# Kernel tuning notes

Hardware: AMD Instinct MI355X
Metric: run time of the kernel (lower is better)

Reference implementation:

```python
import jax, jax.numpy as jnp
import numpy as np

N_TOTAL = 2_000_000
B = 50_000
D_MODEL = 128
HIDDEN = 64


def setup_inputs() -> dict:
    key = jax.random.key(0)
    ks = jax.random.split(key, 5)
    h = jax.random.normal(ks[0], (N_TOTAL, D_MODEL), dtype=jnp.float32)
    segment_ids = jnp.sort(jax.random.randint(ks[1], (N_TOTAL,), 0, B, dtype=jnp.int32))
    # MLP params (Linear stores [out,in] in torch; we use [in,out] with x @ W)
    W1 = jax.random.normal(ks[2], (D_MODEL, HIDDEN), dtype=jnp.float32) * (1.0 / np.sqrt(D_MODEL))
    b1 = jnp.zeros((HIDDEN,), dtype=jnp.float32)
    W2 = jax.random.normal(ks[3], (HIDDEN, HIDDEN), dtype=jnp.float32) * (1.0 / np.sqrt(HIDDEN))
    b2 = jnp.zeros((HIDDEN,), dtype=jnp.float32)
    W3 = jax.random.normal(ks[4], (HIDDEN, 1), dtype=jnp.float32) * (1.0 / np.sqrt(HIDDEN))
    b3 = jnp.zeros((1,), dtype=jnp.float32)
    return {"h": h, "segment_ids": segment_ids, "num_segments": B,
            "W1": W1, "b1": b1, "W2": W2, "b2": b2, "W3": W3, "b3": b3}


def reference(h, segment_ids, num_segments, W1, b1, W2, b2, W3, b3):
    # Ragged mean pooling over atoms -> [B, d_model] (fused segment reduce)
    sums = jax.ops.segment_sum(h, segment_ids, num_segments=num_segments)
    counts = jax.ops.segment_sum(jnp.ones((h.shape[0],), h.dtype), segment_ids,
                                 num_segments=num_segments)
    pooled = sums / jnp.maximum(counts, 1.0)[:, None]  # [B, d_model]
    # 3-layer MLP with SiLU -> scalar per molecule
    x = jax.nn.silu(pooled @ W1 + b1)
    x = jax.nn.silu(x @ W2 + b2)
    scalar = (x @ W3 + b3)[:, 0]  # [B]
    return scalar
```

## Files before the change

kernel.cpp:

```cpp
#include <hip/hip_runtime.h>

#define D_MODEL 128
#define HIDDEN 64
#define WPB 8
#define NTHREADS (WPB * 64)
#define NBLOCKS 512
#define W1_STRIDE 132
#define W2_STRIDE 68

__global__ void seg_bounds_kernel(const int* __restrict__ seg, int n, int B,
                                  int* __restrict__ seg_start) {
  int i = blockIdx.x * blockDim.x + threadIdx.x;
  if (i >= n) return;
  int s = seg[i];
  if (i == 0) {
    for (int t = 0; t <= s; ++t) seg_start[t] = 0;
  } else {
    int p = seg[i - 1];
    for (int t = p + 1; t <= s; ++t) seg_start[t] = i;
  }
  if (i == n - 1) {
    for (int t = s + 1; t <= B; ++t) seg_start[t] = n;
  }
}

__device__ __forceinline__ float silu(float x) {
  return x / (1.0f + __expf(-x));
}

__global__ __launch_bounds__(NTHREADS, 4) void pool_mlp_kernel(
    const float* __restrict__ h, const int* __restrict__ seg_start,
    const float* __restrict__ W1, const float* __restrict__ b1,
    const float* __restrict__ W2, const float* __restrict__ b2,
    const float* __restrict__ W3, const float* __restrict__ b3,
    float* __restrict__ out, int B) {
  __shared__ float sW1T[HIDDEN * W1_STRIDE];
  __shared__ float sW2T[HIDDEN * W2_STRIDE];
  __shared__ float pooled_lds[WPB][D_MODEL];
  __shared__ float x1_lds[WPB][HIDDEN];

  const int tid = threadIdx.x;

#pragma unroll
  for (int i = tid; i < (D_MODEL * HIDDEN) / 4; i += NTHREADS) {
    float4 v = reinterpret_cast<const float4*>(W1)[i];
    int k = i >> 4;
    int j = (4 * i) & (HIDDEN - 1);
    sW1T[(j + 0) * W1_STRIDE + k] = v.x;
    sW1T[(j + 1) * W1_STRIDE + k] = v.y;
    sW1T[(j + 2) * W1_STRIDE + k] = v.z;
    sW1T[(j + 3) * W1_STRIDE + k] = v.w;
  }
#pragma unroll
  for (int i = tid; i < (HIDDEN * HIDDEN) / 4; i += NTHREADS) {
    float4 v = reinterpret_cast<const float4*>(W2)[i];
    int k = i >> 4;
    int j = (4 * i) & (HIDDEN - 1);
    sW2T[(j + 0) * W2_STRIDE + k] = v.x;
    sW2T[(j + 1) * W2_STRIDE + k] = v.y;
    sW2T[(j + 2) * W2_STRIDE + k] = v.z;
    sW2T[(j + 3) * W2_STRIDE + k] = v.w;
  }
  __syncthreads();

  const int wave = tid >> 6;
  const int lane = tid & 63;

  const float b1l = b1[lane];
  const float b2l = b2[lane];
  const float w3l = W3[lane];
  const float b3l = b3[0];

  const int G = gridDim.x * WPB;
  const int g = blockIdx.x * WPB + wave;
  const int base = B / G;
  const int rem = B - base * G;
  const int my_cnt = base + (g < rem ? 1 : 0);
  const int my_s0 = g * base + (g < rem ? g : rem);
  if (my_cnt == 0) return;

  const int half = lane >> 5;
  const int l32 = lane & 63 & 31;
  const float4* __restrict__ hv = reinterpret_cast<const float4*>(h);
  const float4* __restrict__ pv =
      reinterpret_cast<const float4*>(&pooled_lds[wave][0]);
  const float4* __restrict__ x1v =
      reinterpret_cast<const float4*>(&x1_lds[wave][0]);
  const float4* __restrict__ w1v =
      reinterpret_cast<const float4*>(&sW1T[lane * W1_STRIDE]);
  const float4* __restrict__ w2v =
      reinterpret_cast<const float4*>(&sW2T[lane * W2_STRIDE]);

  int start = seg_start[my_s0];
  for (int si = 0; si < my_cnt; ++si) {
    const int s = my_s0 + si;
    const int end = seg_start[s + 1];
    const int cnt = end - start;

    float4 acc0 = make_float4(0.f, 0.f, 0.f, 0.f);
    float4 acc1 = make_float4(0.f, 0.f, 0.f, 0.f);
    int a = start + half;
    for (; a + 2 < end; a += 4) {
      float4 v0 = hv[a * 32 + l32];
      float4 v1 = hv[(a + 2) * 32 + l32];
      acc0.x += v0.x; acc0.y += v0.y; acc0.z += v0.z; acc0.w += v0.w;
      acc1.x += v1.x; acc1.y += v1.y; acc1.z += v1.z; acc1.w += v1.w;
    }
    if (a < end) {
      float4 v0 = hv[a * 32 + l32];
      acc0.x += v0.x; acc0.y += v0.y; acc0.z += v0.z; acc0.w += v0.w;
    }
    acc0.x += acc1.x; acc0.y += acc1.y; acc0.z += acc1.z; acc0.w += acc1.w;
    acc0.x += __shfl_xor(acc0.x, 32);
    acc0.y += __shfl_xor(acc0.y, 32);
    acc0.z += __shfl_xor(acc0.z, 32);
    acc0.w += __shfl_xor(acc0.w, 32);

    const float inv = 1.0f / (float)max(cnt, 1);
    if (half == 0) {
      float4 p = make_float4(acc0.x * inv, acc0.y * inv,
                             acc0.z * inv, acc0.w * inv);
      reinterpret_cast<float4*>(&pooled_lds[wave][0])[l32] = p;
    }
    __builtin_amdgcn_wave_barrier();

    float a1 = b1l;
#pragma unroll 8
    for (int t = 0; t < D_MODEL / 4; ++t) {
      float4 p = pv[t];
      float4 w = w1v[t];
      a1 = fmaf(p.x, w.x, a1);
      a1 = fmaf(p.y, w.y, a1);
      a1 = fmaf(p.z, w.z, a1);
      a1 = fmaf(p.w, w.w, a1);
    }
    const float x1 = silu(a1);
    x1_lds[wave][lane] = x1;
    __builtin_amdgcn_wave_barrier();

    float a2 = b2l;
#pragma unroll 8
    for (int t = 0; t < HIDDEN / 4; ++t) {
      float4 p = x1v[t];
      float4 w = w2v[t];
      a2 = fmaf(p.x, w.x, a2);
      a2 = fmaf(p.y, w.y, a2);
      a2 = fmaf(p.z, w.z, a2);
      a2 = fmaf(p.w, w.w, a2);
    }
    const float x2 = silu(a2);

    float prod = x2 * w3l;
#pragma unroll
    for (int off = 32; off >= 1; off >>= 1) {
      prod += __shfl_xor(prod, off);
    }
    if (lane == 0) out[s] = prod + b3l;

    start = end;
  }
}

extern "C" void kernel_launch(void* const* d_in, const int* in_sizes, int n_in,
                              void* d_out, int out_size, void* d_ws, size_t ws_size,
                              hipStream_t stream) {
  const float* h = (const float*)d_in[0];
  const int* seg = (const int*)d_in[1];
  const float* W1 = (const float*)d_in[3];
  const float* b1 = (const float*)d_in[4];
  const float* W2 = (const float*)d_in[5];
  const float* b2 = (const float*)d_in[6];
  const float* W3 = (const float*)d_in[7];
  const float* b3 = (const float*)d_in[8];
  float* out = (float*)d_out;

  const int n = in_sizes[1];
  const int B = out_size;

  int* seg_start = (int*)d_ws;

  {
    int threads = 256;
    int blocks = (n + threads - 1) / threads;
    seg_bounds_kernel<<<blocks, threads, 0, stream>>>(seg, n, B, seg_start);
  }
  {
    pool_mlp_kernel<<<NBLOCKS, NTHREADS, 0, stream>>>(
        h, seg_start, W1, b1, W2, b2, W3, b3, out, B);
  }
}
```

Before: 197.2 us.

## Batch four segments per MLP pass and prefetch next batch's atoms

Each wave now pools four segments into LDS, then runs the MLP over all four at once, so every W1/W2 weight read from LDS is reused across four segments. Before the MLP compute, it issues loads for the first atoms of the next batch so global memory latency overlaps the MLP math. The pooling inner loop is also unrolled to four independent float4 loads per iteration. The cost is more registers and LDS per wave, which could lower occupancy, plus clamped tail loads that fetch a few unused rows.

```diff
diff --git a/kernel.cpp b/kernel.cpp
--- a/kernel.cpp
+++ b/kernel.cpp
@@ -7,6 +7,7 @@
 #define NBLOCKS 512
 #define W1_STRIDE 132
 #define W2_STRIDE 68
+#define SEG_BATCH 4
 
 __global__ void seg_bounds_kernel(const int* __restrict__ seg, int n, int B,
                                   int* __restrict__ seg_start) {
@@ -27,17 +28,25 @@
 __device__ __forceinline__ float silu(float x) {
   return x / (1.0f + __expf(-x));
 }
+__device__ __forceinline__ float4 f4add(float4 a, float4 b) {
+  return make_float4(a.x + b.x, a.y + b.y, a.z + b.z, a.w + b.w);
+}
+__device__ __forceinline__ float wave_sum(float p) {
+#pragma unroll
+  for (int off = 32; off >= 1; off >>= 1) p += __shfl_xor(p, off);
+  return p;
+}
 
 __global__ __launch_bounds__(NTHREADS, 4) void pool_mlp_kernel(
     const float* __restrict__ h, const int* __restrict__ seg_start,
     const float* __restrict__ W1, const float* __restrict__ b1,
     const float* __restrict__ W2, const float* __restrict__ b2,
     const float* __restrict__ W3, const float* __restrict__ b3,
-    float* __restrict__ out, int B) {
+    float* __restrict__ out, int B, int n_atoms) {
   __shared__ float sW1T[HIDDEN * W1_STRIDE];
   __shared__ float sW2T[HIDDEN * W2_STRIDE];
-  __shared__ float pooled_lds[WPB][D_MODEL];
-  __shared__ float x1_lds[WPB][HIDDEN];
+  __shared__ float pooled_lds[WPB][SEG_BATCH][D_MODEL];
+  __shared__ float x1_lds[WPB][SEG_BATCH][HIDDEN];
 
   const int tid = threadIdx.x;
 
@@ -65,7 +74,6 @@
 
   const int wave = tid >> 6;
   const int lane = tid & 63;
-
   const float b1l = b1[lane];
   const float b2l = b2[lane];
   const float w3l = W3[lane];
@@ -80,84 +88,129 @@
   if (my_cnt == 0) return;
 
   const int half = lane >> 5;
-  const int l32 = lane & 63 & 31;
+  const int l32 = lane & 31;
   const float4* __restrict__ hv = reinterpret_cast<const float4*>(h);
-  const float4* __restrict__ pv =
-      reinterpret_cast<const float4*>(&pooled_lds[wave][0]);
-  const float4* __restrict__ x1v =
-      reinterpret_cast<const float4*>(&x1_lds[wave][0]);
   const float4* __restrict__ w1v =
       reinterpret_cast<const float4*>(&sW1T[lane * W1_STRIDE]);
   const float4* __restrict__ w2v =
       reinterpret_cast<const float4*>(&sW2T[lane * W2_STRIDE]);
 
+  float4 pf0, pf1, pf2, pf3;
+  bool have_pf = false;
+
   int start = seg_start[my_s0];
-  for (int si = 0; si < my_cnt; ++si) {
-    const int s = my_s0 + si;
-    const int end = seg_start[s + 1];
-    const int cnt = end - start;
-
-    float4 acc0 = make_float4(0.f, 0.f, 0.f, 0.f);
-    float4 acc1 = make_float4(0.f, 0.f, 0.f, 0.f);
-    int a = start + half;
-    for (; a + 2 < end; a += 4) {
-      float4 v0 = hv[a * 32 + l32];
-      float4 v1 = hv[(a + 2) * 32 + l32];
-      acc0.x += v0.x; acc0.y += v0.y; acc0.z += v0.z; acc0.w += v0.w;
-      acc1.x += v1.x; acc1.y += v1.y; acc1.z += v1.z; acc1.w += v1.w;
-    }
-    if (a < end) {
-      float4 v0 = hv[a * 32 + l32];
-      acc0.x += v0.x; acc0.y += v0.y; acc0.z += v0.z; acc0.w += v0.w;
-    }
-    acc0.x += acc1.x; acc0.y += acc1.y; acc0.z += acc1.z; acc0.w += acc1.w;
-    acc0.x += __shfl_xor(acc0.x, 32);
-    acc0.y += __shfl_xor(acc0.y, 32);
-    acc0.z += __shfl_xor(acc0.z, 32);
-    acc0.w += __shfl_xor(acc0.w, 32);
-
-    const float inv = 1.0f / (float)max(cnt, 1);
-    if (half == 0) {
-      float4 p = make_float4(acc0.x * inv, acc0.y * inv,
-                             acc0.z * inv, acc0.w * inv);
-      reinterpret_cast<float4*>(&pooled_lds[wave][0])[l32] = p;
+  for (int si = 0; si < my_cnt; si += SEG_BATCH) {
+    const int nb = min(SEG_BATCH, my_cnt - si);
+
+    for (int b = 0; b < nb; ++b) {
+      const int end = seg_start[my_s0 + si + b + 1];
+      const int cnt = end - start;
+      float4 acc0 = make_float4(0.f, 0.f, 0.f, 0.f);
+      float4 acc1 = acc0, acc2 = acc0, acc3 = acc0;
+      int a = start + half;
+      if (have_pf) {
+        if (a < end) acc0 = f4add(acc0, pf0);
+        if (a + 2 < end) acc1 = f4add(acc1, pf1);
+        if (a + 4 < end) acc2 = f4add(acc2, pf2);
+        if (a + 6 < end) acc3 = f4add(acc3, pf3);
+        a += 8;
+        have_pf = false;
+      }
+      for (; a + 6 < end; a += 8) {
+        float4 v0 = hv[(a + 0) * 32 + l32];
+        float4 v1 = hv[(a + 2) * 32 + l32];
+        float4 v2 = hv[(a + 4) * 32 + l32];
+        float4 v3 = hv[(a + 6) * 32 + l32];
+        acc0 = f4add(acc0, v0);
+        acc1 = f4add(acc1, v1);
+        acc2 = f4add(acc2, v2);
+        acc3 = f4add(acc3, v3);
+      }
+      if (a < end) {
+        const int c1 = min(a + 2, n_atoms - 1);
+        const int c2 = min(a + 4, n_atoms - 1);
+        float4 v0 = hv[a * 32 + l32];
+        float4 v1 = hv[c1 * 32 + l32];
+        float4 v2 = hv[c2 * 32 + l32];
+        acc0 = f4add(acc0, v0);
+        if (a + 2 < end) acc1 = f4add(acc1, v1);
+        if (a + 4 < end) acc2 = f4add(acc2, v2);
+      }
+      acc0 = f4add(f4add(acc0, acc1), f4add(acc2, acc3));
+      acc0.x += __shfl_xor(acc0.x, 32);
+      acc0.y += __shfl_xor(acc0.y, 32);
+      acc0.z += __shfl_xor(acc0.z, 32);
+      acc0.w += __shfl_xor(acc0.w, 32);
+      const float inv = 1.0f / (float)max(cnt, 1);
+      if (half == 0) {
+        reinterpret_cast<float4*>(&pooled_lds[wave][b][0])[l32] = make_float4(
+            acc0.x * inv, acc0.y * inv, acc0.z * inv, acc0.w * inv);
+      }
+      start = end;
     }
     __builtin_amdgcn_wave_barrier();
 
-    float a1 = b1l;
+    if (si + SEG_BATCH < my_cnt) {
+      const int pa = start + half;
+      const int c0 = min(pa + 0, n_atoms - 1);
+      const int c1 = min(pa + 2, n_atoms - 1);
+      const int c2 = min(pa + 4, n_atoms - 1);
+      const int c3 = min(pa + 6, n_atoms - 1);
+      pf0 = hv[c0 * 32 + l32];
+      pf1 = hv[c1 * 32 + l32];
+      pf2 = hv[c2 * 32 + l32];
+      pf3 = hv[c3 * 32 + l32];
+      have_pf = true;
+    }
+
+    const float4* pv0 = reinterpret_cast<const float4*>(&pooled_lds[wave][0][0]);
+    const float4* pv1 = reinterpret_cast<const float4*>(&pooled_lds[wave][1][0]);
+    const float4* pv2 = reinterpret_cast<const float4*>(&pooled_lds[wave][2][0]);
+    const float4* pv3 = reinterpret_cast<const float4*>(&pooled_lds[wave][3][0]);
+    float a1b0 = b1l, a1b1 = b1l, a1b2 = b1l, a1b3 = b1l;
 #pragma unroll 8
     for (int t = 0; t < D_MODEL / 4; ++t) {
-      float4 p = pv[t];
       float4 w = w1v[t];
-      a1 = fmaf(p.x, w.x, a1);
-      a1 = fmaf(p.y, w.y, a1);
-      a1 = fmaf(p.z, w.z, a1);
-      a1 = fmaf(p.w, w.w, a1);
-    }
-    const float x1 = silu(a1);
-    x1_lds[wave][lane] = x1;
+      float4 p0 = pv0[t], p1 = pv1[t], p2 = pv2[t], p3 = pv3[t];
+      a1b0 = fmaf(p0.x, w.x, a1b0); a1b0 = fmaf(p0.y, w.y, a1b0);
+      a1b0 = fmaf(p0.z, w.z, a1b0); a1b0 = fmaf(p0.w, w.w, a1b0);
+      a1b1 = fmaf(p1.x, w.x, a1b1); a1b1 = fmaf(p1.y, w.y, a1b1);
+      a1b1 = fmaf(p1.z, w.z, a1b1); a1b1 = fmaf(p1.w, w.w, a1b1);
+      a1b2 = fmaf(p2.x, w.x, a1b2); a1b2 = fmaf(p2.y, w.y, a1b2);
+      a1b2 = fmaf(p2.z, w.z, a1b2); a1b2 = fmaf(p2.w, w.w, a1b2);
+      a1b3 = fmaf(p3.x, w.x, a1b3); a1b3 = fmaf(p3.y, w.y, a1b3);
+      a1b3 = fmaf(p3.z, w.z, a1b3); a1b3 = fmaf(p3.w, w.w, a1b3);
+    }
+    x1_lds[wave][0][lane] = silu(a1b0);
+    x1_lds[wave][1][lane] = silu(a1b1);
+    x1_lds[wave][2][lane] = silu(a1b2);
+    x1_lds[wave][3][lane] = silu(a1b3);
     __builtin_amdgcn_wave_barrier();
 
-    float a2 = b2l;
+    const float4* x10 = reinterpret_cast<const float4*>(&x1_lds[wave][0][0]);
+    const float4* x11 = reinterpret_cast<const float4*>(&x1_lds[wave][1][0]);
+    const float4* x12 = reinterpret_cast<const float4*>(&x1_lds[wave][2][0]);
+    const float4* x13 = reinterpret_cast<const float4*>(&x1_lds[wave][3][0]);
+    float a2b0 = b2l, a2b1 = b2l, a2b2 = b2l, a2b3 = b2l;
 #pragma unroll 8
     for (int t = 0; t < HIDDEN / 4; ++t) {
-      float4 p = x1v[t];
       float4 w = w2v[t];
-      a2 = fmaf(p.x, w.x, a2);
-      a2 = fmaf(p.y, w.y, a2);
-      a2 = fmaf(p.z, w.z, a2);
-      a2 = fmaf(p.w, w.w, a2);
-    }
-    const float x2 = silu(a2);
-
-    float prod = x2 * w3l;
-#pragma unroll
-    for (int off = 32; off >= 1; off >>= 1) {
-      prod += __shfl_xor(prod, off);
-    }
-    if (lane == 0) out[s] = prod + b3l;
-
-    start = end;
+      float4 p0 = x10[t], p1 = x11[t], p2 = x12[t], p3 = x13[t];
+      a2b0 = fmaf(p0.x, w.x, a2b0); a2b0 = fmaf(p0.y, w.y, a2b0);
+      a2b0 = fmaf(p0.z, w.z, a2b0); a2b0 = fmaf(p0.w, w.w, a2b0);
+      a2b1 = fmaf(p1.x, w.x, a2b1); a2b1 = fmaf(p1.y, w.y, a2b1);
+      a2b1 = fmaf(p1.z, w.z, a2b1); a2b1 = fmaf(p1.w, w.w, a2b1);
+      a2b2 = fmaf(p2.x, w.x, a2b2); a2b2 = fmaf(p2.y, w.y, a2b2);
+      a2b2 = fmaf(p2.z, w.z, a2b2); a2b2 = fmaf(p2.w, w.w, a2b2);
+      a2b3 = fmaf(p3.x, w.x, a2b3); a2b3 = fmaf(p3.y, w.y, a2b3);
+      a2b3 = fmaf(p3.z, w.z, a2b3); a2b3 = fmaf(p3.w, w.w, a2b3);
+    }
+    float r0 = wave_sum(silu(a2b0) * w3l);
+    float r1 = wave_sum(silu(a2b1) * w3l);
+    float r2 = wave_sum(silu(a2b2) * w3l);
+    float r3 = wave_sum(silu(a2b3) * w3l);
+    float val = (lane == 0) ? r0 : (lane == 1) ? r1 : (lane == 2) ? r2 : r3;
+    if (lane < nb) out[my_s0 + si + lane] = val + b3l;
   }
 }
 
@@ -186,6 +239,6 @@
   }
   {
     pool_mlp_kernel<<<NBLOCKS, NTHREADS, 0, stream>>>(
-        h, seg_start, W1, b1, W2, b2, W3, b3, out, B);
-  }
-}
+        h, seg_start, W1, b1, W2, b2, W3, b3, out, B, n);
+  }
+}
```

New measurement: 199.0 us. About the same (+0.9%).
